# Kernel tuning notes

Measured on AMD Instinct MI355X. Metric: run time of the kernel, lower is better.

The kernel has to match this reference:

```python
import jax, jax.numpy as jnp
import numpy as np

B, L, E, K = 64, 1024, 256, 8  # batch, seq_len, d_model, topk (slice width)


def setup_inputs() -> dict:
    key = jax.random.key(0)
    ks = jax.random.split(key, 5)
    s = 1.0 / np.sqrt(E).astype(np.float32)
    return {
        "series": jax.random.normal(ks[0], (B, L, E), jnp.float32),
        "text_series": jax.random.normal(ks[1], (B, L, E), jnp.float32),
        "Wq": jax.random.normal(ks[2], (E, E), jnp.float32) * s,
        "bq": jnp.zeros((E,), jnp.float32),
        "Wk": jax.random.normal(ks[3], (E, E), jnp.float32) * s,
        "bk": jnp.zeros((E,), jnp.float32),
        "Wv": jax.random.normal(ks[4], (E, E), jnp.float32) * s,
        "bv": jnp.zeros((E,), jnp.float32),
    }


def reference(series, text_series, Wq, bq, Wk, bk, Wv, bv):
    Bn, Ln, En = series.shape
    scale = 1.0 / np.sqrt(En).astype(np.float32)
    # nn.Linear: x @ W.T + b
    q = series @ Wq.T + bq            # (B, L, E)
    k = text_series @ Wk.T + bk       # (B, L, E)
    v = text_series @ Wv.T + bv       # (B, L, E)
    # FFT cross-correlation along time axis
    qf = jnp.fft.rfft(q.transpose(0, 2, 1), axis=-1)  # (B, E, L//2+1)
    kf = jnp.fft.rfft(k.transpose(0, 2, 1), axis=-1)
    corr = jnp.fft.irfft(qf * jnp.conj(kf), n=Ln, axis=-1)  # (B, E, L)
    mean_value = corr.mean(axis=1)                           # (B, L)
    # torch.topk(mean over batch, seq_len) == full descending sort of lags
    idx = jnp.argsort(-mean_value.mean(axis=0))              # (L,)
    weights = mean_value[:, idx]                             # (B, L), sorted by lag score
    tmp_corr = jax.nn.softmax(weights * scale, axis=-1)      # (B, L)
    # Original builds cc = concat_i [roll(v, -idx[i], 1) * tmp_corr[:, i]] over all L lags
    # (shape (B, L, L*E)), then returns (cc[..., :K], cc[..., -K:]).
    # With K <= E those slices come solely from the first (i=0) and last (i=L-1) lag blocks.
    out1 = jnp.roll(v, -idx[0], axis=1)[..., :K] * tmp_corr[:, 0][:, None, None]
    out2 = jnp.roll(v, -idx[-1], axis=1)[..., -K:] * tmp_corr[:, -1][:, None, None]
    return (out1, out2)
```

## Files before the change

### kernel.cpp

```cpp
#include <hip/hip_runtime.h>
#include <hip/hip_bf16.h>
#include <math.h>

#define BB 64
#define LL 1024
#define EE 256
#define KK 8
#define EPB 8
#define CHUNKS (EE/EPB)

typedef __attribute__((ext_vector_type(8))) short  bfrag;
typedef __attribute__((ext_vector_type(4))) short  short4v;
typedef __attribute__((ext_vector_type(4))) float  f32x4;

#define MT_KB 10240

#define O_MHI    ((size_t)0)
#define O_MLO    ((size_t)40960)
#define O_BVAUG  ((size_t)81920)
#define O_X      ((size_t)81984)
#define O_KPT    (O_X + (size_t)16777216)
#define O_VSUB   (O_KPT + (size_t)16777216)
#define O_MV     (O_VSUB + (size_t)1048576)
#define O_STATS  (O_MV + (size_t)65536)

__device__ __forceinline__ float2 cmulf(float2 a, float2 b) {
    return make_float2(a.x * b.x - a.y * b.y, a.x * b.y + a.y * b.x);
}

__device__ __forceinline__ int PHY(int i) { return i + (i >> 4); }

__device__ __forceinline__ void splitbf(float x, unsigned short& h, unsigned short& l) {
    __hip_bfloat16 hb = __float2bfloat16(x);
    float hf = __bfloat162float(hb);
    __hip_bfloat16 lb = __float2bfloat16(x - hf);
    h = *(unsigned short*)&hb;
    l = *(unsigned short*)&lb;
}

__device__ __forceinline__ void gload16(const unsigned short* g, unsigned short* l) {
    __builtin_amdgcn_global_load_lds(
        (const __attribute__((address_space(1))) unsigned int*)g,
        (__attribute__((address_space(3))) unsigned int*)l, 16, 0, 0);
}

__device__ __forceinline__ int slot_of(int r, int kq) { return (kq + (r >> 1)) & 3; }

__global__ __launch_bounds__(256) void build_maug(
    const float* __restrict__ Wq, const float* __restrict__ Wk,
    const float* __restrict__ Wv, const float* __restrict__ bv,
    unsigned short* __restrict__ mhiT, unsigned short* __restrict__ mloT,
    float* __restrict__ bvaug) {
    int n = blockIdx.x;
    int j = threadIdx.x;
    float acc;
    if (n < EE) {
        acc = 0.f;
        for (int e = 0; e < EE; ++e)
            acc += Wq[e * EE + n] * Wk[e * EE + j];
    } else {
        int t = n - EE;
        int c = (t < 8) ? t : (240 + t);
        acc = Wv[c * EE + j];
    }
    unsigned short h, l;
    splitbf(acc, h, l);
    const int kb = j >> 5, kq = (j >> 3) & 3;
    const size_t dst = (size_t)kb * MT_KB + n * 32 + slot_of(n, kq) * 8 + (j & 7);
    mhiT[dst] = h;
    mloT[dst] = l;
    if (n == 0 && j < 16) bvaug[j] = bv[(j < 8) ? j : (240 + j)];
}

__global__ __launch_bounds__(256) void split_T(
    const float* __restrict__ T,
    unsigned short* __restrict__ thiT, unsigned short* __restrict__ tloT) {
    const size_t g = (size_t)blockIdx.x * 256 + threadIdx.x;
    const size_t i = g * 8;
    const int s = (int)(i >> 8), k = (int)(i & 255);
    const int kb = k >> 5, kq = (k >> 3) & 3;
    const int st = s >> 6, row = s & 63;
    f32x4 v0 = *(const f32x4*)&T[i];
    f32x4 v1 = *(const f32x4*)&T[i + 4];
    short4v h0, l0, h1, l1;
#pragma unroll
    for (int j = 0; j < 4; ++j) {
        unsigned short h, l;
        splitbf(v0[j], h, l); h0[j] = (short)h; l0[j] = (short)l;
        splitbf(v1[j], h, l); h1[j] = (short)h; l1[j] = (short)l;
    }
    const size_t dst = ((size_t)(st * 8 + kb)) * 2048 + row * 32 + slot_of(row, kq) * 8;
    *(short4v*)&thiT[dst] = h0; *(short4v*)&thiT[dst + 4] = h1;
    *(short4v*)&tloT[dst] = l0; *(short4v*)&tloT[dst + 4] = l1;
}

__global__ __launch_bounds__(256) void transpose_S(
    const float* __restrict__ S, float* __restrict__ St) {
    __shared__ float tile[64][65];
    const int b = blockIdx.z;
    const int l0 = blockIdx.x * 64, e0 = blockIdx.y * 64;
    const int tx = threadIdx.x & 15, ty = threadIdx.x >> 4;
#pragma unroll
    for (int r = 0; r < 4; ++r) {
        const int lr = ty + 16 * r;
        f32x4 v = *(const f32x4*)&S[((size_t)b * LL + l0 + lr) * EE + e0 + tx * 4];
#pragma unroll
        for (int i = 0; i < 4; ++i) tile[lr][tx * 4 + i] = v[i];
    }
    __syncthreads();
#pragma unroll
    for (int r = 0; r < 4; ++r) {
        const int er = ty + 16 * r;
        f32x4 v;
#pragma unroll
        for (int i = 0; i < 4; ++i) v[i] = tile[tx * 4 + i][er];
        *(f32x4*)&St[((size_t)b * EE + e0 + er) * LL + l0 + tx * 4] = v;
    }
}

__global__ __launch_bounds__(256, 3) void gemm_mfma(
    const unsigned short* __restrict__ thiT, const unsigned short* __restrict__ tloT,
    const unsigned short* __restrict__ mhiT, const unsigned short* __restrict__ mloT,
    const float* __restrict__ bvaug,
    float* __restrict__ kp_t, float* __restrict__ vsub) {
    __shared__ alignas(16) unsigned short Ah[2048];
    __shared__ alignas(16) unsigned short Al[2048];
    __shared__ alignas(16) unsigned short Bh[10240];
    __shared__ alignas(16) unsigned short Bl[10240];
    const int tid = threadIdx.x;
    const int w = tid >> 6, lane = tid & 63;
    const int lrow = lane & 15, lk = lane >> 4;
    const int st = blockIdx.x;
    const size_t s0 = (size_t)st * 64;
    const int bb = (int)(s0 >> 10), l0 = (int)(s0 & 1023);
    const int gl = w * 64 + lane;

    f32x4 acc[4][4];
    f32x4 acc2[4];
#pragma unroll
    for (int m = 0; m < 4; ++m) {
#pragma unroll
        for (int c = 0; c < 4; ++c) acc[m][c] = (f32x4){0.f, 0.f, 0.f, 0.f};
        acc2[m] = (f32x4){0.f, 0.f, 0.f, 0.f};
    }

    for (int kb = 0; kb < 8; ++kb) {
        __syncthreads();
        const unsigned short* asrcH = thiT + ((size_t)(st * 8 + kb)) * 2048;
        const unsigned short* asrcL = tloT + ((size_t)(st * 8 + kb)) * 2048;
        gload16(asrcH + gl * 8, &Ah[(size_t)w * 512]);
        gload16(asrcL + gl * 8, &Al[(size_t)w * 512]);
        const unsigned short* bsrcH = mhiT + (size_t)kb * MT_KB;
        const unsigned short* bsrcL = mloT + (size_t)kb * MT_KB;
#pragma unroll
        for (int q = 0; q < 5; ++q)
            gload16(bsrcH + q * 2048 + gl * 8, &Bh[q * 2048 + w * 512]);
#pragma unroll
        for (int q = 0; q < 5; ++q)
            gload16(bsrcL + q * 2048 + gl * 8, &Bl[q * 2048 + w * 512]);
        __syncthreads();

        bfrag ah[4], al[4];
#pragma unroll
        for (int m = 0; m < 4; ++m) {
            const int row = m * 16 + lrow;
            const int off = row * 32 + slot_of(row, lk) * 8;
            ah[m] = *(const bfrag*)&Ah[off];
            al[m] = *(const bfrag*)&Al[off];
        }
#pragma unroll
        for (int c = 0; c < 4; ++c) {
            const int n = w * 64 + c * 16 + lrow;
            const int off = n * 32 + slot_of(n, lk) * 8;
            bfrag bh = *(const bfrag*)&Bh[off];
            bfrag bl = *(const bfrag*)&Bl[off];
#pragma unroll
            for (int m = 0; m < 4; ++m) {
                acc[m][c] = __builtin_amdgcn_mfma_f32_16x16x32_bf16(ah[m], bh, acc[m][c], 0, 0, 0);
                acc[m][c] = __builtin_amdgcn_mfma_f32_16x16x32_bf16(ah[m], bl, acc[m][c], 0, 0, 0);
                acc[m][c] = __builtin_amdgcn_mfma_f32_16x16x32_bf16(al[m], bh, acc[m][c], 0, 0, 0);
            }
        }
        if (w == 0) {
            const int n = EE + lrow;
            const int off = n * 32 + slot_of(n, lk) * 8;
            bfrag bh = *(const bfrag*)&Bh[off];
            bfrag bl = *(const bfrag*)&Bl[off];
#pragma unroll
            for (int m = 0; m < 4; ++m) {
                acc2[m] = __builtin_amdgcn_mfma_f32_16x16x32_bf16(ah[m], bh, acc2[m], 0, 0, 0);
                acc2[m] = __builtin_amdgcn_mfma_f32_16x16x32_bf16(ah[m], bl, acc2[m], 0, 0, 0);
                acc2[m] = __builtin_amdgcn_mfma_f32_16x16x32_bf16(al[m], bh, acc2[m], 0, 0, 0);
            }
        }
    }
#pragma unroll
    for (int m = 0; m < 4; ++m) {
        const int srow = m * 16 + lk * 4;
#pragma unroll
        for (int c = 0; c < 4; ++c) {
            const int n = w * 64 + c * 16 + lrow;
            *(f32x4*)&kp_t[((size_t)(bb * EE + n)) * LL + l0 + srow] = acc[m][c];
        }
    }
    if (w == 0) {
        const float bvv = bvaug[lrow];
#pragma unroll
        for (int m = 0; m < 4; ++m) {
            const int srow = m * 16 + lk * 4;
#pragma unroll
            for (int j = 0; j < 4; ++j)
                vsub[(s0 + srow + j) * 16 + lrow] = acc2[m][j] + bvv;
        }
    }
}

template<bool INV>
__device__ __forceinline__ void fft1024_r4_tail(float2* a, float2* b, int tid) {
    float2* src = a;
    float2* dst = b;
#pragma unroll
    for (int t = 1; t < 5; ++t) {
        const int Ns = 1 << (2 * t);
        __syncthreads();
        const int j = tid;
        const int k = j & (Ns - 1);
        float sv, cv;
        __sincosf(-3.14159265358979323846f * (float)k / (float)(2 * Ns), &sv, &cv);
        float2 w1 = make_float2(cv, sv);
        float2 w2 = cmulf(w1, w1);
        float2 w3 = cmulf(w1, w2);
        if (INV) { w1.y = -w1.y; w2.y = -w2.y; w3.y = -w3.y; }
        float2 a0 = src[PHY(j)];
        float2 a1 = cmulf(w1, src[PHY(j + 256)]);
        float2 a2 = cmulf(w2, src[PHY(j + 512)]);
        float2 a3 = cmulf(w3, src[PHY(j + 768)]);
        float2 t0 = make_float2(a0.x + a2.x, a0.y + a2.y);
        float2 t1 = make_float2(a0.x - a2.x, a0.y - a2.y);
        float2 t2 = make_float2(a1.x + a3.x, a1.y + a3.y);
        float2 t3 = make_float2(a1.x - a3.x, a1.y - a3.y);
        float2 u3 = INV ? make_float2(-t3.y, t3.x) : make_float2(t3.y, -t3.x);
        const int base = ((j >> (2 * t)) << (2 * t + 2)) + k;
        dst[PHY(base)]          = make_float2(t0.x + t2.x, t0.y + t2.y);
        dst[PHY(base + Ns)]     = make_float2(t1.x + u3.x, t1.y + u3.y);
        dst[PHY(base + 2 * Ns)] = make_float2(t0.x - t2.x, t0.y - t2.y);
        dst[PHY(base + 3 * Ns)] = make_float2(t1.x - u3.x, t1.y - u3.y);
        float2* tmp = src; src = dst; dst = tmp;
    }
    __syncthreads();
}

template<bool INV>
__device__ __forceinline__ void fft1024_r4(float2* a, float2* b, int tid) {
    float2* src = a;
    float2* dst = b;
#pragma unroll
    for (int t = 0; t < 5; ++t) {
        const int Ns = 1 << (2 * t);
        __syncthreads();
        const int j = tid;
        const int k = j & (Ns - 1);
        float sv, cv;
        __sincosf(-3.14159265358979323846f * (float)k / (float)(2 * Ns), &sv, &cv);
        float2 w1 = make_float2(cv, sv);
        float2 w2 = cmulf(w1, w1);
        float2 w3 = cmulf(w1, w2);
        if (INV) { w1.y = -w1.y; w2.y = -w2.y; w3.y = -w3.y; }
        float2 a0 = src[PHY(j)];
        float2 a1 = cmulf(w1, src[PHY(j + 256)]);
        float2 a2 = cmulf(w2, src[PHY(j + 512)]);
        float2 a3 = cmulf(w3, src[PHY(j + 768)]);
        float2 t0 = make_float2(a0.x + a2.x, a0.y + a2.y);
        float2 t1 = make_float2(a0.x - a2.x, a0.y - a2.y);
        float2 t2 = make_float2(a1.x + a3.x, a1.y + a3.y);
        float2 t3 = make_float2(a1.x - a3.x, a1.y - a3.y);
        float2 u3 = INV ? make_float2(-t3.y, t3.x) : make_float2(t3.y, -t3.x);
        const int base = ((j >> (2 * t)) << (2 * t + 2)) + k;
        dst[PHY(base)]          = make_float2(t0.x + t2.x, t0.y + t2.y);
        dst[PHY(base + Ns)]     = make_float2(t1.x + u3.x, t1.y + u3.y);
        dst[PHY(base + 2 * Ns)] = make_float2(t0.x - t2.x, t0.y - t2.y);
        dst[PHY(base + 3 * Ns)] = make_float2(t1.x - u3.x, t1.y - u3.y);
        float2* tmp = src; src = dst; dst = tmp;
    }
    __syncthreads();
}

__global__ __launch_bounds__(256) void xcorr_kernel(
    float* __restrict__ St, const float* __restrict__ kp_t) {
    __shared__ float2 bufA[1088];
    __shared__ float2 bufB[1088];
    const int tid = threadIdx.x;
    const int b = blockIdx.x / CHUNKS;
    const int chunk = blockIdx.x % CHUNKS;

    float2 p0 = make_float2(0.f, 0.f);
    float2 p1 = make_float2(0.f, 0.f);
    float px2 = 0.f;

    const size_t base = ((size_t)b * EE + (size_t)chunk * EPB) * LL;
    for (int ee = 0; ee < EPB; ++ee) {
        const size_t rbase = base + (size_t)ee * LL;
        __syncthreads();
        {
            float2 z0 = make_float2(St[rbase + tid],        kp_t[rbase + tid]);
            float2 z1 = make_float2(St[rbase + tid + 256],  kp_t[rbase + tid + 256]);
            float2 z2 = make_float2(St[rbase + tid + 512],  kp_t[rbase + tid + 512]);
            float2 z3 = make_float2(St[rbase + tid + 768],  kp_t[rbase + tid + 768]);
            float2 t0 = make_float2(z0.x + z2.x, z0.y + z2.y);
            float2 t1 = make_float2(z0.x - z2.x, z0.y - z2.y);
            float2 t2 = make_float2(z1.x + z3.x, z1.y + z3.y);
            float2 t3 = make_float2(z1.x - z3.x, z1.y - z3.y);
            float2 u3 = make_float2(t3.y, -t3.x);
            const int q = 4 * tid;
            bufA[PHY(q)]     = make_float2(t0.x + t2.x, t0.y + t2.y);
            bufA[PHY(q + 1)] = make_float2(t1.x + u3.x, t1.y + u3.y);
            bufA[PHY(q + 2)] = make_float2(t0.x - t2.x, t0.y - t2.y);
            bufA[PHY(q + 3)] = make_float2(t1.x - u3.x, t1.y - u3.y);
        }
        fft1024_r4_tail<false>(bufA, bufB, tid);
        {
            float2 A = bufA[PHY(tid)];
            float2 C = bufA[PHY((1024 - tid) & 1023)];
            p0.x += 0.5f * (A.x * C.y + A.y * C.x);
            p0.y += 0.25f * ((A.x * A.x + A.y * A.y) - (C.x * C.x + C.y * C.y));
        }
        {
            int f = tid + 256;
            float2 A = bufA[PHY(f)];
            float2 C = bufA[PHY(1024 - f)];
            p1.x += 0.5f * (A.x * C.y + A.y * C.x);
            p1.y += 0.25f * ((A.x * A.x + A.y * A.y) - (C.x * C.x + C.y * C.y));
        }
        if (tid == 0) {
            float2 A = bufA[PHY(512)];
            px2 += A.x * A.y;
        }
    }
    float2* pp = (float2*)&St[base];
    pp[tid] = p0;
    pp[tid + 256] = p1;
    if (tid == 0) pp[512] = make_float2(px2, 0.f);
}

__global__ __launch_bounds__(256) void ifft_kernel(
    const float* __restrict__ St, float* __restrict__ mv) {
    __shared__ float2 bufA[1088];
    __shared__ float2 bufB[1088];
    const int tid = threadIdx.x;
    const int b = blockIdx.x;
#pragma unroll
    for (int u = 0; u < 2; ++u) {
        int f = tid + (u << 8);
        float2 s = make_float2(0.f, 0.f);
        for (int c = 0; c < CHUNKS; ++c) {
            const float2* pp = (const float2*)&St[((size_t)b * EE + (size_t)c * EPB) * LL];
            float2 v = pp[f];
            s.x += v.x; s.y += v.y;
        }
        if (f == 0) s.y = 0.f;
        bufA[PHY(f)] = s;
        if (f > 0) bufA[PHY(1024 - f)] = make_float2(s.x, -s.y);
    }
    if (tid == 0) {
        float sx = 0.f;
        for (int c = 0; c < CHUNKS; ++c) {
            const float2* pp = (const float2*)&St[((size_t)b * EE + (size_t)c * EPB) * LL];
            sx += pp[512].x;
        }
        bufA[PHY(512)] = make_float2(sx, 0.f);
    }
    fft1024_r4<true>(bufA, bufB, tid);
    const float sc = 1.f / (1024.f * 256.f);
#pragma unroll
    for (int u = 0; u < 4; ++u) {
        int t = tid + (u << 8);
        mv[(size_t)b * LL + t] = bufB[PHY(t)].x * sc;
    }
}

__global__ __launch_bounds__(1024) void argidx_kernel(
    const float* __restrict__ mv, int* __restrict__ istats) {
    __shared__ float smax[1024], smin[1024];
    __shared__ int imax[1024], imin[1024];
    const int t = threadIdx.x;
    float g = 0.f;
    for (int b = 0; b < BB; ++b) g += mv[(size_t)b * LL + t];
    smax[t] = g; smin[t] = g; imax[t] = t; imin[t] = t;
    __syncthreads();
    for (int s = 512; s > 0; s >>= 1) {
        if (t < s) {
            if (smax[t + s] > smax[t] ||
                (smax[t + s] == smax[t] && imax[t + s] < imax[t])) {
                smax[t] = smax[t + s]; imax[t] = imax[t + s];
            }
            if (smin[t + s] < smin[t] ||
                (smin[t + s] == smin[t] && imin[t + s] > imin[t])) {
                smin[t] = smin[t + s]; imin[t] = imin[t + s];
            }
        }
        __syncthreads();
    }
    if (t == 0) { istats[0] = imax[0]; istats[1] = imin[0]; }
}

__global__ __launch_bounds__(256) void softmax_kernel(
    const float* __restrict__ mv, const int* __restrict__ istats,
    float* __restrict__ w01) {
    __shared__ float red[256];
    const int b = blockIdx.x, t = threadIdx.x;
    const float scale = 0.0625f;
    const float* row = mv + (size_t)b * LL;
    float m = -INFINITY;
    for (int i = t; i < LL; i += 256) m = fmaxf(m, row[i]);
    red[t] = m; __syncthreads();
    for (int s = 128; s > 0; s >>= 1) {
        if (t < s) red[t] = fmaxf(red[t], red[t + s]);
        __syncthreads();
    }
    m = red[0]; __syncthreads();
    float sum = 0.f;
    for (int i = t; i < LL; i += 256) sum += expf((row[i] - m) * scale);
    red[t] = sum; __syncthreads();
    for (int s = 128; s > 0; s >>= 1) {
        if (t < s) red[t] += red[t + s];
        __syncthreads();
    }
    if (t == 0) {
        float denom = red[0];
        w01[b]      = expf((row[istats[0]] - m) * scale) / denom;
        w01[BB + b] = expf((row[istats[1]] - m) * scale) / denom;
    }
}

__global__ __launch_bounds__(256) void out_kernel(
    const float* __restrict__ vsub, const int* __restrict__ istats,
    const float* __restrict__ w01, float* __restrict__ out) {
    const int i = blockIdx.x * 256 + threadIdx.x;
    const int half = (i >= BB * LL * KK) ? 1 : 0;
    const int j = i - half * BB * LL * KK;
    const int b = j / (LL * KK);
    const int rem = j % (LL * KK);
    const int l = rem / KK, kk = rem % KK;
    const int sh = istats[half];
    const int lr = (l + sh) & (LL - 1);
    const float w = w01[half * BB + b];
    out[i] = vsub[(size_t)(b * LL + lr) * 16 + half * 8 + kk] * w;
}

extern "C" void kernel_launch(void* const* d_in, const int* in_sizes, int n_in,
                              void* d_out, int out_size, void* d_ws, size_t ws_size,
                              hipStream_t stream) {
    const float* S  = (const float*)d_in[0];
    const float* T  = (const float*)d_in[1];
    const float* Wq = (const float*)d_in[2];
    const float* Wk = (const float*)d_in[4];
    const float* Wv = (const float*)d_in[6];
    const float* bv = (const float*)d_in[7];

    float* ws    = (float*)d_ws;
    unsigned short* mhiT = (unsigned short*)(ws + O_MHI);
    unsigned short* mloT = (unsigned short*)(ws + O_MLO);
    float* bvaug = ws + O_BVAUG;
    unsigned short* thiT = (unsigned short*)(ws + O_X);
    unsigned short* tloT = (unsigned short*)(ws + O_X + 8388608);
    float* st    = ws + O_X;
    float* kp_t  = ws + O_KPT;
    float* vsub  = ws + O_VSUB;
    float* mv    = ws + O_MV;
    float* stats = ws + O_STATS;
    int*   istats = (int*)stats;
    float* w01    = stats + 8;

    build_maug<<<272, 256, 0, stream>>>(Wq, Wk, Wv, bv, mhiT, mloT, bvaug);
    split_T<<<(BB * LL * EE) / (256 * 8), 256, 0, stream>>>(T, thiT, tloT);
    gemm_mfma<<<(BB * LL) / 64, 256, 0, stream>>>(thiT, tloT, mhiT, mloT, bvaug, kp_t, vsub);
    dim3 gT(LL / 64, EE / 64, BB);
    transpose_S<<<gT, 256, 0, stream>>>(S, st);
    xcorr_kernel<<<BB * CHUNKS, 256, 0, stream>>>(st, kp_t);
    ifft_kernel<<<BB, 256, 0, stream>>>(st, mv);
    argidx_kernel<<<1, 1024, 0, stream>>>(mv, istats);
    softmax_kernel<<<BB, 256, 0, stream>>>(mv, istats, w01);
    out_kernel<<<(2 * BB * LL * KK) / 256, 256, 0, stream>>>(vsub, istats, w01, (float*)d_out);
}
```

Baseline: 163.3 us.

## Enlarge GEMM block to 128 rows with 8 waves sharing the weight tile

The projection GEMM now processes 128 sequence rows per block with 512 threads. The waves are split into two row halves and four column groups, so each weight (B) tile staged in shared memory is reused by twice as many rows. The per-k-block B stride is padded from 10240 to 12288 elements so the tile can be loaded in even 512-element chunks by 8 waves, and the workspace offsets shift to match. This roughly halves global weight traffic per output row, in exchange for more shared memory and registers per block, lower occupancy and half as many blocks.

New measurement: 176.2 us. 7.9% more time.

```diff
diff --git a/kernel.cpp b/kernel.cpp
--- a/kernel.cpp
+++ b/kernel.cpp
@@ -13,12 +13,12 @@
 typedef __attribute__((ext_vector_type(4))) short  short4v;
 typedef __attribute__((ext_vector_type(4))) float  f32x4;
 
-#define MT_KB 10240
+#define MT_KB 12288
 
 #define O_MHI    ((size_t)0)
-#define O_MLO    ((size_t)40960)
-#define O_BVAUG  ((size_t)81920)
-#define O_X      ((size_t)81984)
+#define O_MLO    ((size_t)49152)
+#define O_BVAUG  ((size_t)98304)
+#define O_X      ((size_t)98368)
 #define O_KPT    (O_X + (size_t)16777216)
 #define O_VSUB   (O_KPT + (size_t)16777216)
 #define O_MV     (O_VSUB + (size_t)1048576)
@@ -118,22 +118,22 @@
     }
 }
 
-__global__ __launch_bounds__(256, 3) void gemm_mfma(
+__global__ __launch_bounds__(512, 4) void gemm_mfma(
     const unsigned short* __restrict__ thiT, const unsigned short* __restrict__ tloT,
     const unsigned short* __restrict__ mhiT, const unsigned short* __restrict__ mloT,
     const float* __restrict__ bvaug,
     float* __restrict__ kp_t, float* __restrict__ vsub) {
-    __shared__ alignas(16) unsigned short Ah[2048];
-    __shared__ alignas(16) unsigned short Al[2048];
-    __shared__ alignas(16) unsigned short Bh[10240];
-    __shared__ alignas(16) unsigned short Bl[10240];
+    __shared__ alignas(16) unsigned short Ah[4096];
+    __shared__ alignas(16) unsigned short Al[4096];
+    __shared__ alignas(16) unsigned short Bh[12288];
+    __shared__ alignas(16) unsigned short Bl[12288];
     const int tid = threadIdx.x;
     const int w = tid >> 6, lane = tid & 63;
+    const int mh = w >> 2, wn = w & 3;
     const int lrow = lane & 15, lk = lane >> 4;
-    const int st = blockIdx.x;
-    const size_t s0 = (size_t)st * 64;
+    const int st2 = (int)blockIdx.x * 2;
+    const size_t s0 = (size_t)blockIdx.x * 128;
     const int bb = (int)(s0 >> 10), l0 = (int)(s0 & 1023);
-    const int gl = w * 64 + lane;
 
     f32x4 acc[4][4];
     f32x4 acc2[4];
@@ -146,31 +146,34 @@
 
     for (int kb = 0; kb < 8; ++kb) {
         __syncthreads();
-        const unsigned short* asrcH = thiT + ((size_t)(st * 8 + kb)) * 2048;
-        const unsigned short* asrcL = tloT + ((size_t)(st * 8 + kb)) * 2048;
-        gload16(asrcH + gl * 8, &Ah[(size_t)w * 512]);
-        gload16(asrcL + gl * 8, &Al[(size_t)w * 512]);
-        const unsigned short* bsrcH = mhiT + (size_t)kb * MT_KB;
-        const unsigned short* bsrcL = mloT + (size_t)kb * MT_KB;
-#pragma unroll
-        for (int q = 0; q < 5; ++q)
-            gload16(bsrcH + q * 2048 + gl * 8, &Bh[q * 2048 + w * 512]);
-#pragma unroll
-        for (int q = 0; q < 5; ++q)
-            gload16(bsrcL + q * 2048 + gl * 8, &Bl[q * 2048 + w * 512]);
+        {
+            const size_t tsel = (size_t)((st2 + (w >> 2)) * 8 + kb) * 2048 + (w & 3) * 512;
+            gload16(thiT + tsel + lane * 8, &Ah[w * 512]);
+            gload16(tloT + tsel + lane * 8, &Al[w * 512]);
+        }
+        {
+            const unsigned short* bsrcH = mhiT + (size_t)kb * MT_KB;
+            const unsigned short* bsrcL = mloT + (size_t)kb * MT_KB;
+#pragma unroll
+            for (int q = 0; q < 3; ++q) {
+                const int ch = q * 8 + w;
+                gload16(bsrcH + ch * 512 + lane * 8, &Bh[ch * 512]);
+                gload16(bsrcL + ch * 512 + lane * 8, &Bl[ch * 512]);
+            }
+        }
         __syncthreads();
 
         bfrag ah[4], al[4];
 #pragma unroll
         for (int m = 0; m < 4; ++m) {
-            const int row = m * 16 + lrow;
-            const int off = row * 32 + slot_of(row, lk) * 8;
+            const int rr = m * 16 + lrow;
+            const int off = mh * 2048 + rr * 32 + slot_of(rr, lk) * 8;
             ah[m] = *(const bfrag*)&Ah[off];
             al[m] = *(const bfrag*)&Al[off];
         }
 #pragma unroll
         for (int c = 0; c < 4; ++c) {
-            const int n = w * 64 + c * 16 + lrow;
+            const int n = wn * 64 + c * 16 + lrow;
             const int off = n * 32 + slot_of(n, lk) * 8;
             bfrag bh = *(const bfrag*)&Bh[off];
             bfrag bl = *(const bfrag*)&Bl[off];
@@ -181,7 +184,7 @@
                 acc[m][c] = __builtin_amdgcn_mfma_f32_16x16x32_bf16(al[m], bh, acc[m][c], 0, 0, 0);
             }
         }
-        if (w == 0) {
+        if (wn == 0) {
             const int n = EE + lrow;
             const int off = n * 32 + slot_of(n, lk) * 8;
             bfrag bh = *(const bfrag*)&Bh[off];
@@ -196,18 +199,18 @@
     }
 #pragma unroll
     for (int m = 0; m < 4; ++m) {
-        const int srow = m * 16 + lk * 4;
+        const int srow = mh * 64 + m * 16 + lk * 4;
 #pragma unroll
         for (int c = 0; c < 4; ++c) {
-            const int n = w * 64 + c * 16 + lrow;
+            const int n = wn * 64 + c * 16 + lrow;
             *(f32x4*)&kp_t[((size_t)(bb * EE + n)) * LL + l0 + srow] = acc[m][c];
         }
     }
-    if (w == 0) {
+    if (wn == 0) {
         const float bvv = bvaug[lrow];
 #pragma unroll
         for (int m = 0; m < 4; ++m) {
-            const int srow = m * 16 + lk * 4;
+            const int srow = mh * 64 + m * 16 + lk * 4;
 #pragma unroll
             for (int j = 0; j < 4; ++j)
                 vsub[(s0 + srow + j) * 16 + lrow] = acc2[m][j] + bvv;
@@ -473,7 +476,7 @@
 
     build_maug<<<272, 256, 0, stream>>>(Wq, Wk, Wv, bv, mhiT, mloT, bvaug);
     split_T<<<(BB * LL * EE) / (256 * 8), 256, 0, stream>>>(T, thiT, tloT);
-    gemm_mfma<<<(BB * LL) / 64, 256, 0, stream>>>(thiT, tloT, mhiT, mloT, bvaug, kp_t, vsub);
+    gemm_mfma<<<(BB * LL) / 128, 512, 0, stream>>>(thiT, tloT, mhiT, mloT, bvaug, kp_t, vsub);
     dim3 gT(LL / 64, EE / 64, BB);
     transpose_S<<<gT, 256, 0, stream>>>(S, st);
     xcorr_kernel<<<BB * CHUNKS, 256, 0, stream>>>(st, kp_t);
```

## Double-buffer A tiles and shrink padded B weight chunk in MFMA GEMM

Applied to the files above, without the earlier changes.

Double-buffers the activation (A) hi/lo tiles in shared memory so the next k-block's A load is issued while the current block computes. It also shrinks the per-k-block weight slab from 5×2048 to 17×512 elements, dropping padding rows and changing the workspace offsets to match. The aim is to hide global-load latency and load fewer bytes per iteration. It costs more A shared memory, and the smaller B layout must match however the host packs the weights.

New measurement: 160.2 us, median of 2. No clear change (-1.9%).

```diff
diff --git a/kernel.cpp b/kernel.cpp
--- a/kernel.cpp
+++ b/kernel.cpp
@@ -13,12 +13,12 @@
 typedef __attribute__((ext_vector_type(4))) short  short4v;
 typedef __attribute__((ext_vector_type(4))) float  f32x4;
 
-#define MT_KB 10240
+#define MT_KB 8704
 
 #define O_MHI    ((size_t)0)
-#define O_MLO    ((size_t)40960)
-#define O_BVAUG  ((size_t)81920)
-#define O_X      ((size_t)81984)
+#define O_MLO    ((size_t)34816)
+#define O_BVAUG  ((size_t)69632)
+#define O_X      ((size_t)69696)
 #define O_KPT    (O_X + (size_t)16777216)
 #define O_VSUB   (O_KPT + (size_t)16777216)
 #define O_MV     (O_VSUB + (size_t)1048576)
@@ -123,17 +123,16 @@
     const unsigned short* __restrict__ mhiT, const unsigned short* __restrict__ mloT,
     const float* __restrict__ bvaug,
     float* __restrict__ kp_t, float* __restrict__ vsub) {
-    __shared__ alignas(16) unsigned short Ah[2048];
-    __shared__ alignas(16) unsigned short Al[2048];
-    __shared__ alignas(16) unsigned short Bh[10240];
-    __shared__ alignas(16) unsigned short Bl[10240];
+    __shared__ alignas(16) unsigned short Ah[4096];
+    __shared__ alignas(16) unsigned short Al[4096];
+    __shared__ alignas(16) unsigned short Bh[8704];
+    __shared__ alignas(16) unsigned short Bl[8704];
     const int tid = threadIdx.x;
     const int w = tid >> 6, lane = tid & 63;
     const int lrow = lane & 15, lk = lane >> 4;
     const int st = blockIdx.x;
     const size_t s0 = (size_t)st * 64;
     const int bb = (int)(s0 >> 10), l0 = (int)(s0 & 1023);
-    const int gl = w * 64 + lane;
 
     f32x4 acc[4][4];
     f32x4 acc2[4];
@@ -144,27 +143,40 @@
         acc2[m] = (f32x4){0.f, 0.f, 0.f, 0.f};
     }
 
+    {
+        const size_t tsel = (size_t)(st * 8 + 0) * 2048 + w * 512;
+        gload16(thiT + tsel + lane * 8, &Ah[w * 512]);
+        gload16(tloT + tsel + lane * 8, &Al[w * 512]);
+    }
+
+#pragma unroll
     for (int kb = 0; kb < 8; ++kb) {
         __syncthreads();
-        const unsigned short* asrcH = thiT + ((size_t)(st * 8 + kb)) * 2048;
-        const unsigned short* asrcL = tloT + ((size_t)(st * 8 + kb)) * 2048;
-        gload16(asrcH + gl * 8, &Ah[(size_t)w * 512]);
-        gload16(asrcL + gl * 8, &Al[(size_t)w * 512]);
         const unsigned short* bsrcH = mhiT + (size_t)kb * MT_KB;
         const unsigned short* bsrcL = mloT + (size_t)kb * MT_KB;
 #pragma unroll
-        for (int q = 0; q < 5; ++q)
-            gload16(bsrcH + q * 2048 + gl * 8, &Bh[q * 2048 + w * 512]);
-#pragma unroll
-        for (int q = 0; q < 5; ++q)
-            gload16(bsrcL + q * 2048 + gl * 8, &Bl[q * 2048 + w * 512]);
-        __syncthreads();
-
+        for (int q = 0; q < 4; ++q) {
+            const int ch = q * 4 + w;
+            gload16(bsrcH + ch * 512 + lane * 8, &Bh[ch * 512]);
+            gload16(bsrcL + ch * 512 + lane * 8, &Bl[ch * 512]);
+        }
+        if (w == 0) {
+            gload16(bsrcH + 16 * 512 + lane * 8, &Bh[16 * 512]);
+            gload16(bsrcL + 16 * 512 + lane * 8, &Bl[16 * 512]);
+        }
+        __syncthreads();
+        if (kb < 7) {
+            const int ab = (kb + 1) & 1;
+            const size_t tsel = (size_t)(st * 8 + kb + 1) * 2048 + w * 512;
+            gload16(thiT + tsel + lane * 8, &Ah[ab * 2048 + w * 512]);
+            gload16(tloT + tsel + lane * 8, &Al[ab * 2048 + w * 512]);
+        }
+        const int ao = (kb & 1) * 2048;
         bfrag ah[4], al[4];
 #pragma unroll
         for (int m = 0; m < 4; ++m) {
             const int row = m * 16 + lrow;
-            const int off = row * 32 + slot_of(row, lk) * 8;
+            const int off = ao + row * 32 + slot_of(row, lk) * 8;
             ah[m] = *(const bfrag*)&Ah[off];
             al[m] = *(const bfrag*)&Al[off];
         }
```
